# Performance work log

Hardware: AMD Instinct MI355X
Metric: run time of the kernel (lower is better)

The kernel has to match this reference:

```python
import jax, jax.numpy as jnp
import numpy as np

B, T, HID = 2, 1024, 2048
H, DK, DV = 16, 128, 128
KC = 4          # short-conv kernel size
CHUNK = 64
EPS = 1e-5


def _dwconv_silu(x, w):
    # causal depthwise conv1d + SiLU: x [B,T,C], w [C,K]
    K = w.shape[1]
    xp = jnp.pad(x, ((0, 0), (K - 1, 0), (0, 0)))
    y = sum(xp[:, i:i + x.shape[1], :] * w[:, i] for i in range(K))
    return jax.nn.silu(y)


def _l2norm(x):
    return x * jax.lax.rsqrt(jnp.sum(x * x, -1, keepdims=True) + 1e-6)


def setup_inputs() -> dict:
    key = jax.random.key(0)
    ks = jax.random.split(key, 22)
    std = 0.02
    w = lambda k, s: jax.random.normal(k, s, jnp.float32) * std
    return dict(
        hidden_states=jax.random.normal(ks[0], (B, T, HID), jnp.float32),
        Wq=w(ks[1], (HID, H * DK)),
        Wk=w(ks[2], (HID, H * DK)),
        Wv=w(ks[3], (HID, H * DV)),
        conv_wq=w(ks[4], (H * DK, KC)),
        conv_wk=w(ks[5], (H * DK, KC)),
        conv_wv=w(ks[6], (H * DV, KC)),
        Wgb1=w(ks[7], (HID, DV)), Wgb2=w(ks[8], (DV, H * DK)),
        Wgd1=w(ks[9], (HID, DV)), Wgd2=w(ks[10], (DV, H * DK)),
        Wbb=w(ks[11], (HID, H)), Wbd=w(ks[12], (HID, H)),
        Wlam=w(ks[13], (HID, H)),
        A_log=jnp.log(jax.random.uniform(ks[14], (H,), jnp.float32, 1.0, 16.0)),
        dt_bias=jnp.zeros((H * DK,), jnp.float32),
        Wg1=w(ks[15], (HID, DV)), Wg2=w(ks[16], (DV, H * DV)),
        bg2=jnp.zeros((H * DV,), jnp.float32),
        onorm_w=jnp.ones((DV,), jnp.float32),
        Wo=w(ks[17], (H * DV, HID)),
    )


def _fkda_core(q, k, v, gf, gs, bf, bs):
    # dual-state (fast/slow) gated delta rule.
    # q,k: [B,T,H,DK]; v: [B,T,H,DV]; gf/gs: log-decay [B,T,H,DK]; bf/bs: [B,T,H]
    scale = DK ** -0.5
    tm = lambda x: jnp.moveaxis(x, 1, 0)                 # time-major
    qT, kT, vT = tm(q) * scale, tm(k), tm(v)
    g2 = jnp.stack([tm(gf), tm(gs)], 1)                  # [T,2,B,H,DK]
    b2 = jnp.stack([tm(bf), tm(bs)], 1)                  # [T,2,B,H]
    NC = T // CHUNK
    chunkify = lambda x: x.reshape((NC, CHUNK) + x.shape[1:])
    inputs = tuple(map(chunkify, (qT, kT, vT, g2, b2)))

    def step(S, inp):
        qt, kt, vt, gt, bt = inp                         # S: [2,B,H,DK,DV]
        S = S * jnp.exp(gt)[..., None]                   # per-channel decay on key dim
        mem = jnp.einsum('bhk,sbhkv->sbhv', kt, S)       # current memory readout
        u = bt[..., None] * (vt[None] - mem)             # delta-rule residual write
        S = S + jnp.einsum('bhk,sbhv->sbhkv', kt, u)
        o = jnp.einsum('bhk,sbhkv->sbhv', qt, S)
        return S, o

    @jax.checkpoint
    def chunk_step(S, inp):
        return jax.lax.scan(step, S, inp)

    S0 = jnp.zeros((2, q.shape[0], H, DK, DV), q.dtype)
    _, o = jax.lax.scan(chunk_step, S0, inputs)          # [NC,CHUNK,2,B,H,DV]
    o = o.reshape((T,) + o.shape[2:])
    return jnp.moveaxis(o[:, 0], 0, 1), jnp.moveaxis(o[:, 1], 0, 1)


def reference(hidden_states, Wq, Wk, Wv, conv_wq, conv_wk, conv_wv,
              Wgb1, Wgb2, Wgd1, Wgd2, Wbb, Wbd, Wlam, A_log, dt_bias,
              Wg1, Wg2, bg2, onorm_w, Wo):
    x = hidden_states
    b, t, _ = x.shape
    q = _dwconv_silu(x @ Wq, conv_wq).reshape(b, t, H, DK)
    k = _dwconv_silu(x @ Wk, conv_wk).reshape(b, t, H, DK)
    v = _dwconv_silu(x @ Wv, conv_wv).reshape(b, t, H, DV)
    g_base = ((x @ Wgb1) @ Wgb2).reshape(b, t, H, DK)    # low-rank decay gates
    g_delta = ((x @ Wgd1) @ Wgd2).reshape(b, t, H, DK)
    bb, bd = x @ Wbb, x @ Wbd
    lam = jax.nn.sigmoid(x @ Wlam)                       # [b,t,H] fast/slow mix
    beta_fast = jax.nn.sigmoid(bb + bd)
    beta_slow = jax.nn.sigmoid(bb - bd)
    dtb = dt_bias.reshape(H, DK)
    gate_of = lambda g: -jnp.exp(A_log)[None, None, :, None] * jax.nn.softplus(g + dtb)
    gf = gate_of(g_base + g_delta)                       # fused_kda_gate, fast
    gs = gate_of(g_base - g_delta)                       # slow (share_decay_gate=False)
    q, k = _l2norm(q), _l2norm(k)                        # use_qk_l2norm_in_kernel
    o_f, o_s = _fkda_core(q, k, v, gf, gs, beta_fast, beta_slow)
    o = lam[..., None] * o_f + (1.0 - lam[..., None]) * o_s
    gate = ((x @ Wg1) @ Wg2 + bg2).reshape(b, t, H, DV)
    o = o * jax.lax.rsqrt(jnp.mean(o * o, -1, keepdims=True) + EPS) * onorm_w
    o = o * jax.nn.sigmoid(gate)                         # FusedRMSNormGated(sigmoid)
    return o.reshape(b, t, H * DV) @ Wo
```

## Files before the change

kernel.cpp:

```cpp
#include <hip/hip_runtime.h>
#include <hip/hip_bf16.h>
#include <math.h>
#include <stdint.h>

#define B_   2
#define T_   1024
#define HID_ 2048
#define H_   16
#define DK_  128
#define DV_  128
#define TS_  16

typedef __bf16 bf16;
typedef __attribute__((ext_vector_type(8))) __bf16 bf16x8;
typedef __attribute__((ext_vector_type(4))) float f32x4;

typedef __attribute__((address_space(3))) uint32_t* lds_ptr_t;
typedef const __attribute__((address_space(1))) uint32_t* glb_ptr_t;

__device__ __forceinline__ float sigmoidf_(float x) {
    return 1.0f / (1.0f + __expf(-x));
}

__device__ __forceinline__ void ldg_to_lds16(const void* g, void* lds) {
    __builtin_amdgcn_global_load_lds((glb_ptr_t)(uintptr_t)g,
                                     (lds_ptr_t)(uintptr_t)lds, 16, 0, 0);
}

template <int CTRL>
__device__ __forceinline__ float dpp_ror_add(float x) {
    int yi = __builtin_amdgcn_update_dpp(
        0, __builtin_bit_cast(int, x), CTRL, 0xF, 0xF, true);
    return x + __builtin_bit_cast(float, yi);
}
__device__ __forceinline__ float row16_allreduce(float x) {
    x = dpp_ror_add<0x128>(x);
    x = dpp_ror_add<0x124>(x);
    x = dpp_ror_add<0x122>(x);
    x = dpp_ror_add<0x121>(x);
    return x;
}

__global__ __launch_bounds__(256) void cast_bf16_kernel(
    const float* __restrict__ in, bf16* __restrict__ out)
{
    int i = blockIdx.x * 256 + threadIdx.x;
    float4 a = ((const float4*)in)[2 * i];
    float4 b = ((const float4*)in)[2 * i + 1];
    bf16x8 o;
    o[0] = (bf16)a.x; o[1] = (bf16)a.y; o[2] = (bf16)a.z; o[3] = (bf16)a.w;
    o[4] = (bf16)b.x; o[5] = (bf16)b.y; o[6] = (bf16)b.z; o[7] = (bf16)b.w;
    ((bf16x8*)out)[i] = o;
}

__global__ __launch_bounds__(256) void tcast_kernel(
    const float* __restrict__ W, bf16* __restrict__ Wt, int K, int N)
{
    __shared__ float tile[32][33];
    const int k0 = blockIdx.y * 32, n0 = blockIdx.x * 32;
    const int r = threadIdx.x >> 5, c = threadIdx.x & 31;
    #pragma unroll
    for (int i = 0; i < 4; ++i)
        tile[r + 8 * i][c] = W[(size_t)(k0 + r + 8 * i) * N + n0 + c];
    __syncthreads();
    #pragma unroll
    for (int i = 0; i < 4; ++i)
        Wt[(size_t)(n0 + r + 8 * i) * K + k0 + c] = (bf16)tile[c][r + 8 * i];
}

__global__ __launch_bounds__(256) void tcast_off_kernel(
    const float* __restrict__ W, bf16* __restrict__ Wt,
    int N, int noff, int koff, float sign)
{
    __shared__ float tile[32][33];
    const int k0 = blockIdx.y * 32, n0 = blockIdx.x * 32;
    const int r = threadIdx.x >> 5, c = threadIdx.x & 31;
    #pragma unroll
    for (int i = 0; i < 4; ++i)
        tile[r + 8 * i][c] = W[(size_t)(k0 + r + 8 * i) * N + n0 + c];
    __syncthreads();
    #pragma unroll
    for (int i = 0; i < 4; ++i)
        Wt[(size_t)(noff + n0 + r + 8 * i) * 256 + koff + k0 + c] =
            (bf16)(sign * tile[c][r + 8 * i]);
}

__global__ __launch_bounds__(256) void mfma_gemm_kernel(
    const bf16* __restrict__ A, const bf16* __restrict__ Bt,
    const float* __restrict__ bias, void* __restrict__ Cout,
    int M, int N, int Kfull, int lda, int ldc, int bf16out)
{
    __shared__ bf16 As[128 * 32];
    __shared__ bf16 Bs[128 * 32];

    const int tid  = threadIdx.x;
    const int w    = tid >> 6;
    const int lane = tid & 63;
    const int n0   = blockIdx.x * 128;
    const int m0   = blockIdx.y * 128;
    const int wm   = (w >> 1) * 64;
    const int wn   = (w & 1) * 64;

    const int lr = lane >> 2;
    const int lc = (lane & 3) * 8;

    f32x4 acc[4][4];
    #pragma unroll
    for (int i = 0; i < 4; ++i)
        #pragma unroll
        for (int j = 0; j < 4; ++j) acc[i][j] = (f32x4)0.0f;

    const bf16* ApL = As + (wm + (lane & 15)) * 32 + (lane >> 4) * 8;
    const bf16* BpL = Bs + (wn + (lane & 15)) * 32 + (lane >> 4) * 8;

    for (int k0 = 0; k0 < Kfull; k0 += 32) {
        #pragma unroll
        for (int i = 0; i < 2; ++i) {
            const int rr = (w * 2 + i) * 16 + lr;
            ldg_to_lds16(A  + (size_t)(m0 + rr) * lda   + k0 + lc, As + (w * 2 + i) * 512);
            ldg_to_lds16(Bt + (size_t)(n0 + rr) * Kfull + k0 + lc, Bs + (w * 2 + i) * 512);
        }
        __syncthreads();

        bf16x8 af[4], bfr[4];
        #pragma unroll
        for (int i = 0; i < 4; ++i) af[i]  = *(const bf16x8*)(ApL + i * 16 * 32);
        #pragma unroll
        for (int j = 0; j < 4; ++j) bfr[j] = *(const bf16x8*)(BpL + j * 16 * 32);
        #pragma unroll
        for (int i = 0; i < 4; ++i)
            #pragma unroll
            for (int j = 0; j < 4; ++j)
                acc[i][j] = __builtin_amdgcn_mfma_f32_16x16x32_bf16(
                    af[i], bfr[j], acc[i][j], 0, 0, 0);
        __syncthreads();
    }

    #pragma unroll
    for (int i = 0; i < 4; ++i) {
        const int row = m0 + wm + i * 16 + (lane >> 4) * 4;
        #pragma unroll
        for (int j = 0; j < 4; ++j) {
            const int col = n0 + wn + j * 16 + (lane & 15);
            const float bv = bias ? bias[col] : 0.0f;
            #pragma unroll
            for (int r = 0; r < 4; ++r) {
                float v = acc[i][j][r] + bv;
                if (bf16out) ((bf16*)Cout)[(size_t)(row + r) * ldc + col] = (bf16)v;
                else ((float*)Cout)[(size_t)(row + r) * ldc + col] = v;
            }
        }
    }
}

__global__ __launch_bounds__(256) void midcast_kernel(
    const float* __restrict__ src, bf16* __restrict__ midb)
{
    int i = blockIdx.x * 256 + threadIdx.x;
    int m = i / 96, c4 = i - m * 96;
    float4 v = *(const float4*)(src + (size_t)m * 6528 + 6144 + c4 * 4);
    bf16 o[4] = {(bf16)v.x, (bf16)v.y, (bf16)v.z, (bf16)v.w};
    *(uint64_t*)(midb + (size_t)m * 384 + c4 * 4) = *(uint64_t*)o;
}

__global__ __launch_bounds__(256) void skinny3_kernel(
    const float* __restrict__ x, const float* __restrict__ Wbb,
    const float* __restrict__ Wbd, const float* __restrict__ Wlam,
    float* __restrict__ bb, float* __restrict__ bd, float* __restrict__ lam)
{
    __shared__ float xs[16][128];
    __shared__ float wsh[128][48];
    const int m0  = blockIdx.x * 16;
    const int tid = threadIdx.x;
    const int r = tid >> 4, cg = tid & 15;
    float acc0 = 0.f, acc1 = 0.f, acc2 = 0.f;

    for (int k0 = 0; k0 < HID_; k0 += 128) {
        __syncthreads();
        #pragma unroll
        for (int i = 0; i < 2; ++i) {
            int f = tid + 256 * i;
            int rr = f >> 5, cc = (f & 31) * 4;
            *(float4*)&xs[rr][cc] = *(const float4*)(x + (size_t)(m0 + rr) * HID_ + k0 + cc);
        }
        #pragma unroll
        for (int i = 0; i < 2; ++i) {
            int f = tid + 256 * i;
            int kk = f >> 2, cc = (f & 3) * 4;
            *(float4*)&wsh[kk][cc]      = *(const float4*)(Wbb  + (size_t)(k0 + kk) * 16 + cc);
            *(float4*)&wsh[kk][16 + cc] = *(const float4*)(Wbd  + (size_t)(k0 + kk) * 16 + cc);
            *(float4*)&wsh[kk][32 + cc] = *(const float4*)(Wlam + (size_t)(k0 + kk) * 16 + cc);
        }
        __syncthreads();
        #pragma unroll 8
        for (int kk = 0; kk < 128; ++kk) {
            float xv = xs[r][kk];
            acc0 += xv * wsh[kk][cg];
            acc1 += xv * wsh[kk][16 + cg];
            acc2 += xv * wsh[kk][32 + cg];
        }
    }
    size_t o = (size_t)(m0 + r) * 16 + cg;
    bb[o] = acc0; bd[o] = acc1; lam[o] = acc2;
}

__global__ __launch_bounds__(256) void conv_silu_kernel(
    const float* __restrict__ xin, int ldx, int coloff,
    const float* __restrict__ w, float* __restrict__ yout, int mode)
{
    const int bt  = blockIdx.x;
    const int t   = bt & (T_ - 1);
    const int tid = threadIdx.x;
    const float* xr = xin + (size_t)bt * ldx + coloff;

    float val[8];
    #pragma unroll
    for (int jj = 0; jj < 8; ++jj) {
        int c = tid + 256 * jj;
        float4 wc = *(const float4*)(w + (size_t)c * 4);
        const float* xc = xr + c;
        float acc = wc.w * xc[0];
        if (t >= 1) acc += wc.z * xc[-ldx];
        if (t >= 2) acc += wc.y * xc[-2 * ldx];
        if (t >= 3) acc += wc.x * xc[-3 * ldx];
        val[jj] = acc * sigmoidf_(acc);
    }

    if (mode > 0) {
        __shared__ float red[4][8];
        const int wv = tid >> 6;
        #pragma unroll
        for (int jj = 0; jj < 8; ++jj) {
            float v2 = val[jj] * val[jj];
            #pragma unroll
            for (int m = 1; m < 64; m <<= 1) v2 += __shfl_xor(v2, m);
            if ((tid & 63) == 0) red[wv][jj] = v2;
        }
        __syncthreads();
        const int wb = (tid >> 7) * 2;
        #pragma unroll
        for (int jj = 0; jj < 8; ++jj) {
            float ss = red[wb][jj] + red[wb + 1][jj];
            float sc = rsqrtf(ss + 1e-6f);
            if (mode == 2) sc *= 0.08838834764831845f;
            val[jj] *= sc;
        }
    }

    const size_t row = (size_t)bt * HID_;
    #pragma unroll
    for (int jj = 0; jj < 8; ++jj)
        yout[row + tid + 256 * jj] = val[jj];
}

__global__ __launch_bounds__(256) void decay_gate_kernel(
    float* gfgs, const float* __restrict__ A_log,
    const float* __restrict__ dt_bias)
{
    size_t i = (size_t)blockIdx.x * 256 + threadIdx.x;
    int c = (int)(i & (HID_ - 1));
    size_t m = i >> 11;
    int h = c >> 7;
    float* pf = gfgs + m * 4096 + c;
    float* ps = pf + 2048;
    float na = -__expf(A_log[h]);
    float db = dt_bias[c];
    float xf = *pf + db;
    float xs = *ps + db;
    float spf = (xf > 20.0f) ? xf : log1pf(__expf(xf));
    float sps = (xs > 20.0f) ? xs : log1pf(__expf(xs));
    *pf = __expf(na * spf);
    *ps = __expf(na * sps);
}

__global__ __launch_bounds__(256) void fkda_kernel(
    const float* __restrict__ qp, const float* __restrict__ kp,
    const float* __restrict__ vp, const float* __restrict__ egf,
    const float* __restrict__ egs, int ldeg,
    const float* __restrict__ bbp, const float* __restrict__ bdp,
    float* __restrict__ ofp, float* __restrict__ osp)
{
    const int bx = blockIdx.x;
    const int bh = bx & 31;
    const int sv = bx >> 5;
    const int b  = bh >> 4;
    const int h  = bh & 15;
    const int s  = sv >> 3;
    const int vc = sv & 7;

    const float* eg = s ? egs : egf;
    float*       op = s ? osp : ofp;
    const float  bsign = s ? -1.0f : 1.0f;

    const int tid  = threadIdx.x;
    const int lane = tid & 63;
    const int w    = tid >> 6;
    const int kseg = lane & 15;
    const int colb = w * 4 + (lane >> 4);

    const size_t base  = (size_t)b * T_ * HID_ + (size_t)h * DK_;
    const size_t baseg = (size_t)b * T_ * ldeg + (size_t)h * DK_;

    __shared__ float EG[TS_ * 128];
    __shared__ float KK[TS_ * 128];
    __shared__ float QQ[TS_ * 128];
    __shared__ float VV[TS_ * 16];
    __shared__ float OT[TS_ * 16];
    __shared__ float BT[TS_];

    float S[8];
    #pragma unroll
    for (int j = 0; j < 8; ++j) S[j] = 0.0f;

    const int l5  = lane & 31;
    const int ttl = lane >> 5;
    const int cg  = (l5 < 16) ? (l5 * 8) : ((l5 - 16) * 8 + 4);
    const int sl  = kseg * 4;

    for (int t0 = 0; t0 < T_; t0 += TS_) {
        #pragma unroll
        for (int i = 0; i < 2; ++i) {
            int n  = w * 2 + i;
            int tt = n * 2 + ttl;
            size_t rq = base  + (size_t)(t0 + tt) * HID_ + cg;
            size_t rg = baseg + (size_t)(t0 + tt) * ldeg + cg;
            ldg_to_lds16(eg + rg, EG + n * 256);
            ldg_to_lds16(kp + rq, KK + n * 256);
            ldg_to_lds16(qp + rq, QQ + n * 256);
        }
        if (tid < 64) {
            int tt = tid >> 2, vo = (tid & 3) * 4;
            size_t g = base + (size_t)(t0 + tt) * HID_ + vc * 16 + vo;
            ((float4*)VV)[tid] = *(const float4*)(vp + g);
        }
        if (tid < TS_) {
            size_t gi = ((size_t)b * T_ + t0 + tid) * H_ + h;
            BT[tid] = sigmoidf_(bbp[gi] + bsign * bdp[gi]);
        }
        __syncthreads();

        #pragma unroll
        for (int tt = 0; tt < TS_; ++tt) {
            float e[8], kf[8], qf[8];
            *(float4*)&e[0]  = *(const float4*)(EG + tt * 128 + sl);
            *(float4*)&e[4]  = *(const float4*)(EG + tt * 128 + 64 + sl);
            *(float4*)&kf[0] = *(const float4*)(KK + tt * 128 + sl);
            *(float4*)&kf[4] = *(const float4*)(KK + tt * 128 + 64 + sl);
            *(float4*)&qf[0] = *(const float4*)(QQ + tt * 128 + sl);
            *(float4*)&qf[4] = *(const float4*)(QQ + tt * 128 + 64 + sl);
            float vcol = VV[tt * 16 + colb];
            float btv  = BT[tt];

            float p0 = 0.0f, p1 = 0.0f;
            #pragma unroll
            for (int j = 0; j < 8; j += 2) {
                S[j]     *= e[j];     p0 += kf[j]     * S[j];
                S[j + 1] *= e[j + 1]; p1 += kf[j + 1] * S[j + 1];
            }
            float p = row16_allreduce(p0 + p1);

            float u = btv * (vcol - p);

            float o0 = 0.0f, o1 = 0.0f;
            #pragma unroll
            for (int j = 0; j < 8; j += 2) {
                S[j]     += kf[j]     * u; o0 += qf[j]     * S[j];
                S[j + 1] += kf[j + 1] * u; o1 += qf[j + 1] * S[j + 1];
            }
            float oo = row16_allreduce(o0 + o1);

            if (kseg == 0) OT[tt * 16 + colb] = oo;
        }
        __syncthreads();

        if (tid < 64) {
            int tt = tid >> 2, vo = (tid & 3) * 4;
            size_t g = base + (size_t)(t0 + tt) * HID_ + vc * 16 + vo;
            *(float4*)(op + g) = ((const float4*)OT)[tid];
        }
    }
}

__global__ __launch_bounds__(256) void mix_norm_gate_kernel(
    const float* of, const float* os, const float* lam_pre,
    const float* gate, const float* onorm_w, bf16* outp)
{
    const int bt  = blockIdx.x;
    const int tid = threadIdx.x;
    const size_t row = (size_t)bt * HID_;

    float val[8];
    #pragma unroll
    for (int jj = 0; jj < 8; ++jj) {
        int c = tid + 256 * jj;
        int h = c >> 7;
        float l = sigmoidf_(lam_pre[(size_t)bt * H_ + h]);
        val[jj] = l * of[row + c] + (1.0f - l) * os[row + c];
    }

    __shared__ float red[4][8];
    const int wv = tid >> 6;
    #pragma unroll
    for (int jj = 0; jj < 8; ++jj) {
        float v2 = val[jj] * val[jj];
        #pragma unroll
        for (int m = 1; m < 64; m <<= 1) v2 += __shfl_xor(v2, m);
        if ((tid & 63) == 0) red[wv][jj] = v2;
    }
    __syncthreads();
    const int wb = (tid >> 7) * 2;
    #pragma unroll
    for (int jj = 0; jj < 8; ++jj) {
        int c = tid + 256 * jj;
        float ss   = red[wb][jj] + red[wb + 1][jj];
        float mean = ss * (1.0f / 128.0f);
        float sc   = rsqrtf(mean + 1e-5f) * onorm_w[c & 127];
        float g    = sigmoidf_(gate[row + c]);
        outp[row + c] = (bf16)(val[jj] * sc * g);
    }
}

extern "C" void kernel_launch(void* const* d_in, const int* in_sizes, int n_in,
                              void* d_out, int out_size, void* d_ws, size_t ws_size,
                              hipStream_t stream) {
    const float* x       = (const float*)d_in[0];
    const float* Wq      = (const float*)d_in[1];
    const float* Wk      = (const float*)d_in[2];
    const float* Wv      = (const float*)d_in[3];
    const float* conv_wq = (const float*)d_in[4];
    const float* conv_wk = (const float*)d_in[5];
    const float* conv_wv = (const float*)d_in[6];
    const float* Wgb1    = (const float*)d_in[7];
    const float* Wgb2    = (const float*)d_in[8];
    const float* Wgd1    = (const float*)d_in[9];
    const float* Wgd2    = (const float*)d_in[10];
    const float* Wbb     = (const float*)d_in[11];
    const float* Wbd     = (const float*)d_in[12];
    const float* Wlam    = (const float*)d_in[13];
    const float* A_log   = (const float*)d_in[14];
    const float* dt_bias = (const float*)d_in[15];
    const float* Wg1     = (const float*)d_in[16];
    const float* Wg2     = (const float*)d_in[17];
    const float* bg2     = (const float*)d_in[18];
    const float* onorm_w = (const float*)d_in[19];
    const float* Wo      = (const float*)d_in[20];
    float* out = (float*)d_out;

    const size_t M = (size_t)B_ * T_;

    float* ws = (float*)d_ws;
    size_t off = 0;
    auto alloc = [&](size_t nfloats) { float* p = ws + off; off += nfloats; return p; };

    float* bufQKV = alloc(M * 6528);
    float* wqkvTf = alloc((size_t)6528 * HID_ / 2);
    float* xbf    = alloc(M * HID_ / 2);
    float* bufQ   = alloc(M * HID_);
    float* bufK   = alloc(M * HID_);
    float* bufV   = alloc(M * HID_);
    float* bufC   = alloc(M * HID_);
    float* bufD   = alloc(M * HID_);
    float* midbf  = alloc(M * 384 / 2);
    float* bb     = alloc(M * H_);
    float* bd     = alloc(M * H_);
    float* lamp   = alloc(M * H_);

    bf16* xb    = (bf16*)xbf;
    bf16* obf   = (bf16*)xbf;
    bf16* wqkvT = (bf16*)wqkvTf;
    bf16* woT   = wqkvT;
    bf16* wcat  = wqkvT + (size_t)HID_ * HID_;
    bf16* wgate = wcat + (size_t)4096 * 256;
    bf16* midb  = (bf16*)midbf;
    float* gfgs = bufQKV;
    float* bufE = bufQKV + M * 4096;

    dim3 blk(256);
    auto gemm = [&](const bf16* A, const bf16* Bt, const float* bias, void* C,
                    int Mm, int Nn, int Kk, int lda, int ldc, int bf16out) {
        dim3 grid(Nn / 128, Mm / 128);
        mfma_gemm_kernel<<<grid, blk, 0, stream>>>(A, Bt, bias, C, Mm, Nn, Kk,
                                                   lda, ldc, bf16out);
    };
    auto tcast = [&](const float* W, bf16* Wt, int Kk, int Nn) {
        tcast_kernel<<<dim3(Nn / 32, Kk / 32), blk, 0, stream>>>(W, Wt, Kk, Nn);
    };

    cast_bf16_kernel<<<dim3((unsigned)(M * HID_ / 8 / 256)), blk, 0, stream>>>(x, xb);

    tcast(Wq,   wqkvT,                          HID_, HID_);
    tcast(Wk,   wqkvT + (size_t)2048 * HID_,    HID_, HID_);
    tcast(Wv,   wqkvT + (size_t)4096 * HID_,    HID_, HID_);
    tcast(Wgb1, wqkvT + (size_t)6144 * HID_,    HID_, 128);
    tcast(Wgd1, wqkvT + (size_t)6272 * HID_,    HID_, 128);
    tcast(Wg1,  wqkvT + (size_t)6400 * HID_,    HID_, 128);
    gemm(xb, wqkvT, nullptr, bufQKV, (int)M, 6528, HID_, HID_, 6528, 0);

    conv_silu_kernel<<<dim3(B_ * T_), blk, 0, stream>>>(bufQKV, 6528, 0,
        conv_wq, bufQ, 2);
    conv_silu_kernel<<<dim3(B_ * T_), blk, 0, stream>>>(bufQKV, 6528, 2048,
        conv_wk, bufK, 1);
    conv_silu_kernel<<<dim3(B_ * T_), blk, 0, stream>>>(bufQKV, 6528, 4096,
        conv_wv, bufV, 0);

    midcast_kernel<<<dim3((unsigned)(M * 96 / 256)), blk, 0, stream>>>(bufQKV, midb);

    skinny3_kernel<<<dim3((unsigned)(M / 16)), blk, 0, stream>>>(
        x, Wbb, Wbd, Wlam, bb, bd, lamp);

    tcast_off_kernel<<<dim3(64, 4), blk, 0, stream>>>(Wgb2, wcat, HID_, 0,    0,   1.0f);
    tcast_off_kernel<<<dim3(64, 4), blk, 0, stream>>>(Wgd2, wcat, HID_, 0,    128, 1.0f);
    tcast_off_kernel<<<dim3(64, 4), blk, 0, stream>>>(Wgb2, wcat, HID_, 2048, 0,   1.0f);
    tcast_off_kernel<<<dim3(64, 4), blk, 0, stream>>>(Wgd2, wcat, HID_, 2048, 128, -1.0f);
    tcast(Wg2, wgate, 128, HID_);
    tcast(Wo,  woT,   HID_, HID_);
    gemm(midb,       wcat,  nullptr, gfgs, (int)M, 4096, 256, 384, 4096, 0);
    gemm(midb + 256, wgate, bg2,     bufE, (int)M, HID_, 128, 384, HID_, 0);

    decay_gate_kernel<<<dim3((unsigned)(M * HID_ / 256)), blk, 0, stream>>>(
        gfgs, A_log, dt_bias);

    fkda_kernel<<<dim3(512), blk, 0, stream>>>(bufQ, bufK, bufV,
        gfgs, gfgs + 2048, 4096, bb, bd, bufC, bufD);

    mix_norm_gate_kernel<<<dim3(B_ * T_), blk, 0, stream>>>(
        bufC, bufD, lamp, bufE, onorm_w, obf);

    gemm(obf, woT, nullptr, out, (int)M, HID_, HID_, HID_, HID_, 0);
}
```

Measured before the change: 746.9 us.

## Double-buffer recurrent scan tiles and prefetch LDS operands into registers

The per-chunk staging of decay, key, query, value and beta tiles is double-buffered in LDS so the next 16-step tile loads while the current one is computed, which drops one barrier per tile. Within a tile, per-step LDS operands are software-pipelined into two register sets so loads overlap the recurrence math. Outputs are written directly to global memory per step instead of through an LDS staging buffer. This doubles LDS use, raises register pressure, and replaces coalesced float4 output stores with scalar stores.

```diff
diff --git a/kernel.cpp b/kernel.cpp
--- a/kernel.cpp
+++ b/kernel.cpp
@@ -273,6 +273,11 @@
     *ps = __expf(na * sps);
 }
 
+struct StepRegs {
+    float4 e0, e1, k0, k1, q0, q1;
+    float v, bt;
+};
+
 __global__ __launch_bounds__(256) void fkda_kernel(
     const float* __restrict__ qp, const float* __restrict__ kp,
     const float* __restrict__ vp, const float* __restrict__ egf,
@@ -300,13 +305,13 @@
 
     const size_t base  = (size_t)b * T_ * HID_ + (size_t)h * DK_;
     const size_t baseg = (size_t)b * T_ * ldeg + (size_t)h * DK_;
-
-    __shared__ float EG[TS_ * 128];
-    __shared__ float KK[TS_ * 128];
-    __shared__ float QQ[TS_ * 128];
-    __shared__ float VV[TS_ * 16];
-    __shared__ float OT[TS_ * 16];
-    __shared__ float BT[TS_];
+    const size_t ocol  = base + (size_t)vc * 16 + colb;
+
+    __shared__ float EG[2][TS_ * 128];
+    __shared__ float KK[2][TS_ * 128];
+    __shared__ float QQ[2][TS_ * 128];
+    __shared__ float VV[2][TS_ * 16];
+    __shared__ float BT[2][TS_];
 
     float S[8];
     #pragma unroll
@@ -317,39 +322,74 @@
     const int cg  = (l5 < 16) ? (l5 * 8) : ((l5 - 16) * 8 + 4);
     const int sl  = kseg * 4;
 
-    for (int t0 = 0; t0 < T_; t0 += TS_) {
+    auto stage_glds = [&](int bi, int t0) {
         #pragma unroll
         for (int i = 0; i < 2; ++i) {
             int n  = w * 2 + i;
             int tt = n * 2 + ttl;
             size_t rq = base  + (size_t)(t0 + tt) * HID_ + cg;
             size_t rg = baseg + (size_t)(t0 + tt) * ldeg + cg;
-            ldg_to_lds16(eg + rg, EG + n * 256);
-            ldg_to_lds16(kp + rq, KK + n * 256);
-            ldg_to_lds16(qp + rq, QQ + n * 256);
+            ldg_to_lds16(eg + rg, &EG[bi][n * 256]);
+            ldg_to_lds16(kp + rq, &KK[bi][n * 256]);
+            ldg_to_lds16(qp + rq, &QQ[bi][n * 256]);
         }
         if (tid < 64) {
-            int tt = tid >> 2, vo = (tid & 3) * 4;
-            size_t g = base + (size_t)(t0 + tt) * HID_ + vc * 16 + vo;
-            ((float4*)VV)[tid] = *(const float4*)(vp + g);
-        }
-        if (tid < TS_) {
-            size_t gi = ((size_t)b * T_ + t0 + tid) * H_ + h;
-            BT[tid] = sigmoidf_(bbp[gi] + bsign * bdp[gi]);
-        }
+            int tt2 = tid >> 2, vo = (tid & 3) * 4;
+            size_t g = base + (size_t)(t0 + tt2) * HID_ + vc * 16 + vo;
+            ldg_to_lds16(vp + g, &VV[bi][0]);
+        }
+    };
+
+    float bbv = 0.0f, bdv = 0.0f;
+    if (tid < TS_) {
+        size_t gi = ((size_t)b * T_ + tid) * H_ + h;
+        bbv = bbp[gi]; bdv = bdp[gi];
+    }
+    stage_glds(0, 0);
+    if (tid < TS_) BT[0][tid] = sigmoidf_(bbv + bsign * bdv);
+
+    for (int t0 = 0; t0 < T_; t0 += TS_) {
+        const int cur = (t0 >> 4) & 1;
+        const int nxt = cur ^ 1;
+        const bool more = (t0 + TS_) < T_;
+
         __syncthreads();
 
-        #pragma unroll
-        for (int tt = 0; tt < TS_; ++tt) {
+        if (more) {
+            stage_glds(nxt, t0 + TS_);
+            if (tid < TS_) {
+                size_t gi = ((size_t)b * T_ + t0 + TS_ + tid) * H_ + h;
+                bbv = bbp[gi]; bdv = bdp[gi];
+            }
+        }
+
+        const float* EGc = EG[cur];
+        const float* KKc = KK[cur];
+        const float* QQc = QQ[cur];
+        const float* VVc = VV[cur];
+        const float* BTc = BT[cur];
+
+        auto ldstep = [&](StepRegs& R, int tt) {
+            const float* Ep = EGc + tt * 128;
+            const float* Kp = KKc + tt * 128;
+            const float* Qp = QQc + tt * 128;
+            R.e0 = *(const float4*)(Ep + sl);
+            R.e1 = *(const float4*)(Ep + 64 + sl);
+            R.k0 = *(const float4*)(Kp + sl);
+            R.k1 = *(const float4*)(Kp + 64 + sl);
+            R.q0 = *(const float4*)(Qp + sl);
+            R.q1 = *(const float4*)(Qp + 64 + sl);
+            R.v  = VVc[tt * 16 + colb];
+            R.bt = BTc[tt];
+        };
+
+        auto compute = [&](const StepRegs& R, int tt) {
             float e[8], kf[8], qf[8];
-            *(float4*)&e[0]  = *(const float4*)(EG + tt * 128 + sl);
-            *(float4*)&e[4]  = *(const float4*)(EG + tt * 128 + 64 + sl);
-            *(float4*)&kf[0] = *(const float4*)(KK + tt * 128 + sl);
-            *(float4*)&kf[4] = *(const float4*)(KK + tt * 128 + 64 + sl);
-            *(float4*)&qf[0] = *(const float4*)(QQ + tt * 128 + sl);
-            *(float4*)&qf[4] = *(const float4*)(QQ + tt * 128 + 64 + sl);
-            float vcol = VV[tt * 16 + colb];
-            float btv  = BT[tt];
+            *(float4*)&e[0]  = R.e0; *(float4*)&e[4]  = R.e1;
+            *(float4*)&kf[0] = R.k0; *(float4*)&kf[4] = R.k1;
+            *(float4*)&qf[0] = R.q0; *(float4*)&qf[4] = R.q1;
+            const float vcol = R.v;
+            const float btv  = R.bt;
 
             float p0 = 0.0f, p1 = 0.0f;
             #pragma unroll
@@ -369,15 +409,20 @@
             }
             float oo = row16_allreduce(o0 + o1);
 
-            if (kseg == 0) OT[tt * 16 + colb] = oo;
-        }
-        __syncthreads();
-
-        if (tid < 64) {
-            int tt = tid >> 2, vo = (tid & 3) * 4;
-            size_t g = base + (size_t)(t0 + tt) * HID_ + vc * 16 + vo;
-            *(float4*)(op + g) = ((const float4*)OT)[tid];
-        }
+            if (kseg == 0) op[ocol + (size_t)(t0 + tt) * HID_] = oo;
+        };
+
+        StepRegs RA, RB;
+        ldstep(RA, 0);
+        #pragma unroll
+        for (int tp = 0; tp < TS_; tp += 2) {
+            ldstep(RB, tp + 1);
+            compute(RA, tp);
+            if (tp + 2 < TS_) ldstep(RA, tp + 2);
+            compute(RB, tp + 1);
+        }
+
+        if (more && tid < TS_) BT[nxt][tid] = sigmoidf_(bbv + bsign * bdv);
     }
 }
 
```

New measurement: 742.1 us. Within noise of the previous version (-0.6%).
